# Performance work log

Measured on AMD Instinct MI355X. Metric: run time of the kernel, lower is better.

The kernel has to match this reference:

```python
import jax, jax.numpy as jnp
import numpy as np

N = 100000
E = 800000
IN_FEATS = 128
H_FEATS = 128
HEADS = 4
OUT = H_FEATS // HEADS  # 32
NEG_SLOPE = 0.2  # DGL GATConv default


def gat_conv(x, src, dst, W, attn_l, attn_r, bias):
    """DGL-style GATConv. x: [N, F_in] -> [N, HEADS, OUT]."""
    h = (x @ W).reshape(N, HEADS, OUT)                      # projected features
    el = jnp.sum(h * attn_l, axis=-1)                       # [N, H]
    er = jnp.sum(h * attn_r, axis=-1)                       # [N, H]
    e = jax.nn.leaky_relu(el[src] + er[dst], NEG_SLOPE)     # [E, H] edge logits
    # edge softmax over incoming edges of each dst node
    m = jax.ops.segment_max(e, dst, num_segments=N)          # [N, H]
    ex = jnp.exp(e - m[dst])                                 # [E, H]
    s = jax.ops.segment_sum(ex, dst, num_segments=N)         # [N, H]
    a = ex / s[dst]                                          # [E, H]
    msg = h[src] * a[:, :, None]                             # [E, H, OUT]
    out = jax.ops.segment_sum(msg, dst, num_segments=N)      # [N, H, OUT]
    return out + bias.reshape(1, HEADS, OUT)


def setup_inputs() -> dict:
    key = jax.random.key(0)
    ks = jax.random.split(key, 12)
    feat = jax.random.normal(ks[0], (N, IN_FEATS), dtype=jnp.float32)
    src = jax.random.randint(ks[1], (E,), 0, N)
    dst = jax.random.randint(ks[2], (E,), 0, N)
    s1 = 1.0 / np.sqrt(IN_FEATS)
    s2 = 1.0 / np.sqrt(H_FEATS)
    return {
        "feat": feat,
        "src": src,
        "dst": dst,
        "W1": jax.random.normal(ks[3], (IN_FEATS, HEADS * OUT), dtype=jnp.float32) * s1,
        "al1": jax.random.normal(ks[4], (HEADS, OUT), dtype=jnp.float32) * s2,
        "ar1": jax.random.normal(ks[5], (HEADS, OUT), dtype=jnp.float32) * s2,
        "b1": jnp.zeros((HEADS * OUT,), dtype=jnp.float32),
        "W2": jax.random.normal(ks[6], (H_FEATS, HEADS * OUT), dtype=jnp.float32) * s2,
        "al2": jax.random.normal(ks[7], (HEADS, OUT), dtype=jnp.float32) * s2,
        "ar2": jax.random.normal(ks[8], (HEADS, OUT), dtype=jnp.float32) * s2,
        "b2": jnp.zeros((HEADS * OUT,), dtype=jnp.float32),
    }


def reference(feat, src, dst, W1, al1, ar1, b1, W2, al2, ar2, b2):
    h = gat_conv(feat, src, dst, W1, al1, ar1, b1).reshape(N, H_FEATS)  # flatten(1)
    h = jax.nn.relu(h)
    h = gat_conv(h, src, dst, W2, al2, ar2, b2).mean(axis=1)            # mean over heads
    return h
```

## Files before the change

### kernel.cpp

```cpp
#include <hip/hip_runtime.h>
#include <math.h>

#define N_NODES 100000
#define N_EDGES 800000
#define NEG_SLOPE 0.2f
#define GEMM_BLOCKS 782
#define HIST_BLOCKS 3125
#define SCAN_BLOCKS 98

typedef __attribute__((ext_vector_type(8))) short short8;
typedef __attribute__((ext_vector_type(4))) float floatx4;

__device__ __forceinline__ float lrelu(float x) { return x > 0.f ? x : NEG_SLOPE * x; }

__device__ __forceinline__ unsigned bf16_rne(float f) {
    unsigned u = __float_as_uint(f);
    return (u + 0x7fffu + ((u >> 16) & 1u)) >> 16;
}
__device__ __forceinline__ unsigned bfpack(float lo, float hi) {
    return bf16_rne(lo) | (bf16_rne(hi) << 16);
}
__device__ __forceinline__ float bflo(unsigned p) { return __uint_as_float(p << 16); }
__device__ __forceinline__ float bfhi(unsigned p) { return __uint_as_float(p & 0xffff0000u); }

__global__ __launch_bounds__(256) void k_prep0(const float* __restrict__ W1,
                                               const float* __restrict__ al1,
                                               const float* __restrict__ ar1,
                                               const float* __restrict__ W2,
                                               const float* __restrict__ al2,
                                               const float* __restrict__ ar2,
                                               unsigned short* __restrict__ wt1,
                                               unsigned short* __restrict__ wt2,
                                               unsigned short* __restrict__ et1,
                                               unsigned short* __restrict__ et2,
                                               int* __restrict__ deg,
                                               int* __restrict__ done) {
    int b = blockIdx.x, tid = threadIdx.x;
    if (b < 128) {
        int t2 = b * 256 + tid;
        const float* W = (t2 < 16384) ? W1 : W2;
        unsigned short* wt = (t2 < 16384) ? wt1 : wt2;
        int t = t2 & 16383;
        int n = t >> 7, k = t & 127;
        wt[t] = (unsigned short)bf16_rne(W[k * 128 + n]);
    } else if (b < 130) {
        const float* W = (b == 128) ? W1 : W2;
        const float* al = (b == 128) ? al1 : al2;
        const float* ar = (b == 128) ? ar1 : ar2;
        unsigned short* et = (b == 128) ? et1 : et2;
        for (int o = tid * 8; o < tid * 8 + 8; o++) {
            int n = o >> 7, k = o & 127;
            float sacc = 0.f;
            if (n < 8) {
                const float* a = (n < 4) ? al : ar;
                int hh = n & 3;
                #pragma unroll 8
                for (int c = 0; c < 32; c++)
                    sacc += W[k * 128 + hh * 32 + c] * a[hh * 32 + c];
            }
            et[n * 128 + k] = (unsigned short)bf16_rne(sacc);
        }
    } else if (b < 228) {
        int i = (b - 130) * 1024 + tid * 4;
        if (i + 3 < N_NODES) *(int4*)&deg[i] = make_int4(0, 0, 0, 0);
        else { for (int j = i; j < N_NODES; j++) if (j >= 0) deg[j] = 0; }
    } else {
        if (tid < 64) done[tid] = 0;
    }
}

__device__ __forceinline__ void gemm_tile(int base, const void* __restrict__ Xv,
                                          const unsigned short* __restrict__ wt,
                                          const unsigned short* __restrict__ et,
                                          unsigned* __restrict__ Hb,
                                          float* __restrict__ EL,
                                          float* __restrict__ ER,
                                          int src_bf16,
                                          unsigned short* wsh,
                                          unsigned short* esh) {
    int tid = threadIdx.x;
    int w = tid >> 6, lane = tid & 63;
    int q = lane >> 4, nl = lane & 15;

    const uint4* wt4 = (const uint4*)wt;
    #pragma unroll
    for (int i = 0; i < 8; i++) {
        int idx = tid + i * 256;
        int rn = idx >> 4, c8 = idx & 15;
        int kc = c8 >> 2, qq = c8 & 3;
        int slot = rn * 128 + ((kc ^ ((rn >> 2) & 3)) * 4 + (qq ^ (rn & 3))) * 8;
        *(uint4*)&wsh[slot] = wt4[idx];
    }
    {
        const uint4* et4 = (const uint4*)et;
        int rn = tid >> 4, c8 = tid & 15;
        *(uint4*)&esh[rn * 136 + c8 * 8] = et4[tid];
    }

    short8 afr[2][4];
    int row0 = base + w * 32 + nl;
    if (!src_bf16) {
        const float4* X4 = (const float4*)Xv;
        #pragma unroll
        for (int rt = 0; rt < 2; rt++) {
            int rr = row0 + rt * 16; if (rr > N_NODES - 1) rr = N_NODES - 1;
            const float4* px = X4 + (size_t)rr * 32 + q * 2;
            #pragma unroll
            for (int kc = 0; kc < 4; kc++) {
                float4 u = px[kc * 8], v = px[kc * 8 + 1];
                short8 f;
                f[0] = (short)bf16_rne(u.x); f[1] = (short)bf16_rne(u.y);
                f[2] = (short)bf16_rne(u.z); f[3] = (short)bf16_rne(u.w);
                f[4] = (short)bf16_rne(v.x); f[5] = (short)bf16_rne(v.y);
                f[6] = (short)bf16_rne(v.z); f[7] = (short)bf16_rne(v.w);
                afr[rt][kc] = f;
            }
        }
    } else {
        const unsigned short* Xb = (const unsigned short*)Xv;
        #pragma unroll
        for (int rt = 0; rt < 2; rt++) {
            int rr = row0 + rt * 16; if (rr > N_NODES - 1) rr = N_NODES - 1;
            #pragma unroll
            for (int kc = 0; kc < 4; kc++)
                afr[rt][kc] = *(const short8*)(Xb + (size_t)rr * 128 + kc * 32 + q * 8);
        }
    }

    floatx4 acc[2][8];
    floatx4 acc_e[2];
    #pragma unroll
    for (int rt = 0; rt < 2; rt++) {
        acc_e[rt] = (floatx4){0.f, 0.f, 0.f, 0.f};
        #pragma unroll
        for (int ct = 0; ct < 8; ct++)
            acc[rt][ct] = (floatx4){0.f, 0.f, 0.f, 0.f};
    }

    __syncthreads();

    int sw_hi = (nl >> 2) & 3, sw_lo = nl & 3;
    #pragma unroll
    for (int ct = 0; ct < 8; ct++) {
        int rbase = (ct * 16 + nl) * 128;
        #pragma unroll
        for (int kc = 0; kc < 4; kc++) {
            short8 b = *(const short8*)&wsh[rbase + ((kc ^ sw_hi) * 4 + (q ^ sw_lo)) * 8];
            acc[0][ct] = __builtin_amdgcn_mfma_f32_16x16x32_bf16(afr[0][kc], b, acc[0][ct], 0, 0, 0);
            acc[1][ct] = __builtin_amdgcn_mfma_f32_16x16x32_bf16(afr[1][kc], b, acc[1][ct], 0, 0, 0);
        }
    }
    #pragma unroll
    for (int kc = 0; kc < 4; kc++) {
        short8 e8 = *(const short8*)&esh[nl * 136 + (kc * 4 + q) * 8];
        acc_e[0] = __builtin_amdgcn_mfma_f32_16x16x32_bf16(afr[0][kc], e8, acc_e[0], 0, 0, 0);
        acc_e[1] = __builtin_amdgcn_mfma_f32_16x16x32_bf16(afr[1][kc], e8, acc_e[1], 0, 0, 0);
    }

    #pragma unroll
    for (int rt = 0; rt < 2; rt++) {
        #pragma unroll
        for (int r = 0; r < 4; r++) {
            int row = base + w * 32 + rt * 16 + q * 4 + r;
            bool valid = row < N_NODES;
            unsigned* hrow = Hb + (size_t)row * 64;
            #pragma unroll
            for (int ct = 0; ct < 8; ct++) {
                float vlo = acc[rt][ct][r];
                float vhi = __shfl_down(vlo, 1);
                if (valid && !(nl & 1)) hrow[ct * 8 + (nl >> 1)] = bfpack(vlo, vhi);
            }
            if (valid && nl < 8) {
                float v = acc_e[rt][r];
                if (nl < 4) EL[row * 4 + nl] = v;
                else        ER[row * 4 + (nl & 3)] = v;
            }
        }
    }
}

__global__ __launch_bounds__(256) void k_gemm_hist(const float* __restrict__ feat,
                                                   const unsigned short* __restrict__ wt1,
                                                   const unsigned short* __restrict__ et1,
                                                   unsigned* __restrict__ Hb,
                                                   float* __restrict__ EL,
                                                   float* __restrict__ ER,
                                                   const int* __restrict__ dst,
                                                   int* __restrict__ deg) {
    __shared__ unsigned short wsh[128 * 128];
    __shared__ unsigned short esh[16 * 136];
    int b = blockIdx.x;
    if (b < GEMM_BLOCKS) {
        gemm_tile(b * 128, feat, wt1, et1, Hb, EL, ER, 0, wsh, esh);
    } else {
        int e = (b - GEMM_BLOCKS) * 256 + threadIdx.x;
        if (e < N_EDGES) atomicAdd(&deg[dst[e]], 1);
    }
}

__global__ __launch_bounds__(256) void k_gemm(const void* __restrict__ Xv,
                                              const unsigned short* __restrict__ wt,
                                              const unsigned short* __restrict__ et,
                                              unsigned* __restrict__ Hb,
                                              float* __restrict__ EL,
                                              float* __restrict__ ER,
                                              int src_bf16) {
    __shared__ unsigned short wsh[128 * 128];
    __shared__ unsigned short esh[16 * 136];
    gemm_tile(blockIdx.x * 128, Xv, wt, et, Hb, EL, ER, src_bf16, wsh, esh);
}

__global__ __launch_bounds__(256) void k_scan_scatter(const int* __restrict__ deg,
                                                      int* __restrict__ rs,
                                                      int* __restrict__ cursor,
                                                      int* __restrict__ bsums,
                                                      int* __restrict__ done,
                                                      const int* __restrict__ src,
                                                      const int* __restrict__ dst,
                                                      int* __restrict__ csr_src) {
    __shared__ int sd[256];
    int tid = threadIdx.x, b = blockIdx.x;
    int base = b * 1024 + tid * 4;
    int v0 = (base + 0 < N_NODES) ? deg[base + 0] : 0;
    int v1 = (base + 1 < N_NODES) ? deg[base + 1] : 0;
    int v2 = (base + 2 < N_NODES) ? deg[base + 2] : 0;
    int v3 = (base + 3 < N_NODES) ? deg[base + 3] : 0;
    int t = v0 + v1 + v2 + v3;
    sd[tid] = t;
    __syncthreads();
    int incl = t;
    for (int off = 1; off < 256; off <<= 1) {
        int x = (tid >= off) ? sd[tid - off] : 0;
        __syncthreads();
        incl += x;
        sd[tid] = incl;
        __syncthreads();
    }
    int excl = incl - t;

    if (tid == 255) {
        atomicExch(&bsums[b], incl);
        __threadfence();
        atomicAdd(&done[0], 1);
    }
    if (tid == 0) {
        while (atomicAdd(&done[0], 0) < SCAN_BLOCKS) { }
    }
    __syncthreads();

    int bv = (tid < b) ? atomicAdd(&bsums[tid], 0) : 0;
    __syncthreads();
    sd[tid] = bv;
    __syncthreads();
    for (int off = 128; off > 0; off >>= 1) {
        if (tid < off) sd[tid] += sd[tid + off];
        __syncthreads();
    }
    int boff = sd[0];

    int p0 = excl + boff;
    if (base + 0 < N_NODES) { rs[base + 0] = p0;                atomicExch(&cursor[base + 0], p0); }
    if (base + 1 < N_NODES) { rs[base + 1] = p0 + v0;           atomicExch(&cursor[base + 1], p0 + v0); }
    if (base + 2 < N_NODES) { rs[base + 2] = p0 + v0 + v1;      atomicExch(&cursor[base + 2], p0 + v0 + v1); }
    if (base + 3 < N_NODES) { rs[base + 3] = p0 + v0 + v1 + v2; atomicExch(&cursor[base + 3], p0 + v0 + v1 + v2); }
    if (b == 0 && tid == 0) rs[N_NODES] = N_EDGES;

    __threadfence();
    __syncthreads();
    if (tid == 0) {
        atomicAdd(&done[1], 1);
        while (atomicAdd(&done[1], 0) < SCAN_BLOCKS) { }
    }
    __syncthreads();

    const int stride = SCAN_BLOCKS * 256;
    int e = b * 256 + tid;
    while (e + 3 * stride < N_EDGES) {
        int d0 = dst[e];             int s0 = src[e];
        int d1 = dst[e + stride];    int s1 = src[e + stride];
        int d2 = dst[e + 2*stride];  int s2 = src[e + 2*stride];
        int d3 = dst[e + 3*stride];  int s3 = src[e + 3*stride];
        int q0 = atomicAdd(&cursor[d0], 1);
        int q1 = atomicAdd(&cursor[d1], 1);
        int q2 = atomicAdd(&cursor[d2], 1);
        int q3 = atomicAdd(&cursor[d3], 1);
        csr_src[q0] = s0;
        csr_src[q1] = s1;
        csr_src[q2] = s2;
        csr_src[q3] = s3;
        e += 4 * stride;
    }
    for (; e < N_EDGES; e += stride) {
        int d = dst[e];
        int p = atomicAdd(&cursor[d], 1);
        csr_src[p] = src[e];
    }
}

__global__ __launch_bounds__(256) void k_gather(const int* __restrict__ rs,
                                                const int* __restrict__ csr_src,
                                                const float* __restrict__ EL,
                                                const float* __restrict__ ER,
                                                const unsigned* __restrict__ Hb,
                                                const float* __restrict__ bias,
                                                void* __restrict__ out,
                                                int final_layer) {
    int wid = (blockIdx.x * blockDim.x + threadIdx.x) >> 6;
    int lane = threadIdx.x & 63;
    int g = lane >> 4, l16 = lane & 15;
    int h = l16 >> 2;
    int n0 = wid * 4;
    if (n0 >= N_NODES) return;
    int nend = min(n0 + 4, N_NODES);

    float bv[8];
    #pragma unroll
    for (int c = 0; c < 8; c++) bv[c] = bias[l16 * 8 + c];

    for (int n = n0; n < nend; n++) {
        int s = rs[n], e = rs[n + 1];
        float erh = ER[n * 4 + h];
        float acc[8];
        #pragma unroll
        for (int c = 0; c < 8; c++) acc[c] = 0.f;
        float sa = 0.f;

        for (int j = s; j < e; j += 8) {
            int j0 = j + g, j1 = j + 4 + g;
            uint4 p0 = make_uint4(0, 0, 0, 0), p1 = make_uint4(0, 0, 0, 0);
            float w0 = 0.f, w1 = 0.f;
            if (j0 < e) {
                int s0 = csr_src[j0];
                p0 = *(const uint4*)(Hb + (size_t)s0 * 64 + l16 * 4);
                w0 = __expf(lrelu(EL[s0 * 4 + h] + erh));
            }
            if (j1 < e) {
                int s1 = csr_src[j1];
                p1 = *(const uint4*)(Hb + (size_t)s1 * 64 + l16 * 4);
                w1 = __expf(lrelu(EL[s1 * 4 + h] + erh));
            }
            sa += w0 + w1;
            acc[0] = fmaf(bflo(p0.x), w0, acc[0]); acc[1] = fmaf(bfhi(p0.x), w0, acc[1]);
            acc[2] = fmaf(bflo(p0.y), w0, acc[2]); acc[3] = fmaf(bfhi(p0.y), w0, acc[3]);
            acc[4] = fmaf(bflo(p0.z), w0, acc[4]); acc[5] = fmaf(bfhi(p0.z), w0, acc[5]);
            acc[6] = fmaf(bflo(p0.w), w0, acc[6]); acc[7] = fmaf(bfhi(p0.w), w0, acc[7]);
            acc[0] = fmaf(bflo(p1.x), w1, acc[0]); acc[1] = fmaf(bfhi(p1.x), w1, acc[1]);
            acc[2] = fmaf(bflo(p1.y), w1, acc[2]); acc[3] = fmaf(bfhi(p1.y), w1, acc[3]);
            acc[4] = fmaf(bflo(p1.z), w1, acc[4]); acc[5] = fmaf(bfhi(p1.z), w1, acc[5]);
            acc[6] = fmaf(bflo(p1.w), w1, acc[6]); acc[7] = fmaf(bfhi(p1.w), w1, acc[7]);
        }

        #pragma unroll
        for (int c = 0; c < 8; c++) {
            acc[c] += __shfl_xor(acc[c], 16);
            acc[c] += __shfl_xor(acc[c], 32);
        }
        sa += __shfl_xor(sa, 16);
        sa += __shfl_xor(sa, 32);
        float inv = (e > s) ? 1.f / sa : 0.f;

        float r[8];
        #pragma unroll
        for (int c = 0; c < 8; c++) r[c] = acc[c] * inv + bv[c];

        if (!final_layer) {
            if (g == 0) {
                uint4 pk;
                pk.x = bfpack(fmaxf(r[0], 0.f), fmaxf(r[1], 0.f));
                pk.y = bfpack(fmaxf(r[2], 0.f), fmaxf(r[3], 0.f));
                pk.z = bfpack(fmaxf(r[4], 0.f), fmaxf(r[5], 0.f));
                pk.w = bfpack(fmaxf(r[6], 0.f), fmaxf(r[7], 0.f));
                *(uint4*)((unsigned*)out + (size_t)n * 64 + l16 * 4) = pk;
            }
        } else {
            #pragma unroll
            for (int c = 0; c < 8; c++) {
                r[c] += __shfl_xor(r[c], 4);
                r[c] += __shfl_xor(r[c], 8);
            }
            if (g == 0 && l16 < 4) {
                float* po = (float*)out + (size_t)n * 32 + l16 * 8;
                *(float4*)po = make_float4(0.25f * r[0], 0.25f * r[1], 0.25f * r[2], 0.25f * r[3]);
                *(float4*)(po + 4) = make_float4(0.25f * r[4], 0.25f * r[5], 0.25f * r[6], 0.25f * r[7]);
            }
        }
    }
}

extern "C" void kernel_launch(void* const* d_in, const int* in_sizes, int n_in,
                              void* d_out, int out_size, void* d_ws, size_t ws_size,
                              hipStream_t stream) {
    const float* feat = (const float*)d_in[0];
    const int* src = (const int*)d_in[1];
    const int* dst = (const int*)d_in[2];
    const float* W1 = (const float*)d_in[3];
    const float* al1 = (const float*)d_in[4];
    const float* ar1 = (const float*)d_in[5];
    const float* b1 = (const float*)d_in[6];
    const float* W2 = (const float*)d_in[7];
    const float* al2 = (const float*)d_in[8];
    const float* ar2 = (const float*)d_in[9];
    const float* b2 = (const float*)d_in[10];
    float* out = (float*)d_out;

    char* ws = (char*)d_ws;
    size_t off = 0;
    auto alloc = [&](size_t bytes) {
        void* p = ws + off;
        off += (bytes + 255) & ~(size_t)255;
        return p;
    };
    int* deg = (int*)alloc((size_t)N_NODES * 4);
    int* done = (int*)alloc(256);
    int* rs = (int*)alloc(((size_t)N_NODES + 1) * 4);
    int* cursor = (int*)alloc((size_t)N_NODES * 4);
    int* bsums = (int*)alloc(128 * 4);
    int* csr_src = (int*)alloc((size_t)N_EDGES * 4);
    unsigned* Hb = (unsigned*)alloc((size_t)N_NODES * 64 * 4);
    float* el = (float*)alloc((size_t)N_NODES * 4 * 4);
    float* er = (float*)alloc((size_t)N_NODES * 4 * 4);
    unsigned* out1b = (unsigned*)alloc((size_t)N_NODES * 64 * 4);
    unsigned short* wt1 = (unsigned short*)alloc(128 * 128 * 2);
    unsigned short* wt2 = (unsigned short*)alloc(128 * 128 * 2);
    unsigned short* et1 = (unsigned short*)alloc(16 * 128 * 2);
    unsigned short* et2 = (unsigned short*)alloc(16 * 128 * 2);

    int gat_blocks = (N_NODES + 15) / 16;

    k_prep0<<<229, 256, 0, stream>>>(W1, al1, ar1, W2, al2, ar2,
                                     wt1, wt2, et1, et2, deg, done);
    k_gemm_hist<<<GEMM_BLOCKS + HIST_BLOCKS, 256, 0, stream>>>(feat, wt1, et1, Hb, el, er,
                                                               dst, deg);
    k_scan_scatter<<<SCAN_BLOCKS, 256, 0, stream>>>(deg, rs, cursor, bsums, done,
                                                    src, dst, csr_src);
    k_gather<<<gat_blocks, 256, 0, stream>>>(rs, csr_src, el, er, Hb, b1, out1b, 0);
    k_gemm<<<GEMM_BLOCKS, 256, 0, stream>>>(out1b, wt2, et2, Hb, el, er, 1);
    k_gather<<<gat_blocks, 256, 0, stream>>>(rs, csr_src, el, er, Hb, b2, out, 1);
}
```

Baseline: 318.9 us.

## Record per-edge rank in histogram pass to drop scatter-phase atomics

The degree-histogram pass now stores each edge's atomicAdd return value as a 16-bit rank, and each thread handles four edges. The scatter phase then computes each CSR position as row_start[dst] + rank with plain loads instead of a second round of atomics on a cursor array, which also removes the cursor array. This trades the contended scatter atomics for an extra 1.6 MB rank write and read. It assumes no node has more than 65535 in-edges.

```diff
diff --git a/kernel.cpp b/kernel.cpp
--- a/kernel.cpp
+++ b/kernel.cpp
@@ -5,7 +5,7 @@
 #define N_EDGES 800000
 #define NEG_SLOPE 0.2f
 #define GEMM_BLOCKS 782
-#define HIST_BLOCKS 3125
+#define HIST4_BLOCKS 782
 #define SCAN_BLOCKS 98
 
 typedef __attribute__((ext_vector_type(8))) short short8;
@@ -186,15 +186,31 @@
                                                    float* __restrict__ EL,
                                                    float* __restrict__ ER,
                                                    const int* __restrict__ dst,
-                                                   int* __restrict__ deg) {
+                                                   int* __restrict__ deg,
+                                                   unsigned short* __restrict__ rank) {
     __shared__ unsigned short wsh[128 * 128];
     __shared__ unsigned short esh[16 * 136];
     int b = blockIdx.x;
     if (b < GEMM_BLOCKS) {
         gemm_tile(b * 128, feat, wt1, et1, Hb, EL, ER, 0, wsh, esh);
     } else {
-        int e = (b - GEMM_BLOCKS) * 256 + threadIdx.x;
-        if (e < N_EDGES) atomicAdd(&deg[dst[e]], 1);
+        int ebase = (b - GEMM_BLOCKS) * 1024 + threadIdx.x;
+        int d[4], c[4];
+        #pragma unroll
+        for (int k = 0; k < 4; k++) {
+            int e = ebase + k * 256;
+            d[k] = (e < N_EDGES) ? dst[e] : 0;
+        }
+        #pragma unroll
+        for (int k = 0; k < 4; k++) {
+            int e = ebase + k * 256;
+            c[k] = (e < N_EDGES) ? atomicAdd(&deg[d[k]], 1) : 0;
+        }
+        #pragma unroll
+        for (int k = 0; k < 4; k++) {
+            int e = ebase + k * 256;
+            if (e < N_EDGES) rank[e] = (unsigned short)c[k];
+        }
     }
 }
 
@@ -212,11 +228,11 @@
 
 __global__ __launch_bounds__(256) void k_scan_scatter(const int* __restrict__ deg,
                                                       int* __restrict__ rs,
-                                                      int* __restrict__ cursor,
                                                       int* __restrict__ bsums,
                                                       int* __restrict__ done,
                                                       const int* __restrict__ src,
                                                       const int* __restrict__ dst,
+                                                      const unsigned short* __restrict__ rank,
                                                       int* __restrict__ csr_src) {
     __shared__ int sd[256];
     int tid = threadIdx.x, b = blockIdx.x;
@@ -259,11 +275,11 @@
     int boff = sd[0];
 
     int p0 = excl + boff;
-    if (base + 0 < N_NODES) { rs[base + 0] = p0;                atomicExch(&cursor[base + 0], p0); }
-    if (base + 1 < N_NODES) { rs[base + 1] = p0 + v0;           atomicExch(&cursor[base + 1], p0 + v0); }
-    if (base + 2 < N_NODES) { rs[base + 2] = p0 + v0 + v1;      atomicExch(&cursor[base + 2], p0 + v0 + v1); }
-    if (base + 3 < N_NODES) { rs[base + 3] = p0 + v0 + v1 + v2; atomicExch(&cursor[base + 3], p0 + v0 + v1 + v2); }
-    if (b == 0 && tid == 0) rs[N_NODES] = N_EDGES;
+    if (base + 0 < N_NODES) atomicExch(&rs[base + 0], p0);
+    if (base + 1 < N_NODES) atomicExch(&rs[base + 1], p0 + v0);
+    if (base + 2 < N_NODES) atomicExch(&rs[base + 2], p0 + v0 + v1);
+    if (base + 3 < N_NODES) atomicExch(&rs[base + 3], p0 + v0 + v1 + v2);
+    if (b == 0 && tid == 0) atomicExch(&rs[N_NODES], N_EDGES);
 
     __threadfence();
     __syncthreads();
@@ -276,24 +292,19 @@
     const int stride = SCAN_BLOCKS * 256;
     int e = b * 256 + tid;
     while (e + 3 * stride < N_EDGES) {
-        int d0 = dst[e];             int s0 = src[e];
-        int d1 = dst[e + stride];    int s1 = src[e + stride];
-        int d2 = dst[e + 2*stride];  int s2 = src[e + 2*stride];
-        int d3 = dst[e + 3*stride];  int s3 = src[e + 3*stride];
-        int q0 = atomicAdd(&cursor[d0], 1);
-        int q1 = atomicAdd(&cursor[d1], 1);
-        int q2 = atomicAdd(&cursor[d2], 1);
-        int q3 = atomicAdd(&cursor[d3], 1);
-        csr_src[q0] = s0;
-        csr_src[q1] = s1;
-        csr_src[q2] = s2;
-        csr_src[q3] = s3;
+        int e1 = e + stride, e2 = e + 2 * stride, e3 = e + 3 * stride;
+        int d0 = dst[e],  d1 = dst[e1], d2 = dst[e2], d3 = dst[e3];
+        int s0 = src[e],  s1 = src[e1], s2 = src[e2], s3 = src[e3];
+        int r0 = rank[e], r1 = rank[e1], r2 = rank[e2], r3 = rank[e3];
+        int q0 = rs[d0], q1 = rs[d1], q2 = rs[d2], q3 = rs[d3];
+        csr_src[q0 + r0] = s0;
+        csr_src[q1 + r1] = s1;
+        csr_src[q2 + r2] = s2;
+        csr_src[q3 + r3] = s3;
         e += 4 * stride;
     }
     for (; e < N_EDGES; e += stride) {
-        int d = dst[e];
-        int p = atomicAdd(&cursor[d], 1);
-        csr_src[p] = src[e];
+        csr_src[rs[dst[e]] + rank[e]] = src[e];
     }
 }
 
@@ -413,8 +424,8 @@
     int* deg = (int*)alloc((size_t)N_NODES * 4);
     int* done = (int*)alloc(256);
     int* rs = (int*)alloc(((size_t)N_NODES + 1) * 4);
-    int* cursor = (int*)alloc((size_t)N_NODES * 4);
     int* bsums = (int*)alloc(128 * 4);
+    unsigned short* rank = (unsigned short*)alloc((size_t)HIST4_BLOCKS * 1024 * 2);
     int* csr_src = (int*)alloc((size_t)N_EDGES * 4);
     unsigned* Hb = (unsigned*)alloc((size_t)N_NODES * 64 * 4);
     float* el = (float*)alloc((size_t)N_NODES * 4 * 4);
@@ -429,10 +440,10 @@
 
     k_prep0<<<229, 256, 0, stream>>>(W1, al1, ar1, W2, al2, ar2,
                                      wt1, wt2, et1, et2, deg, done);
-    k_gemm_hist<<<GEMM_BLOCKS + HIST_BLOCKS, 256, 0, stream>>>(feat, wt1, et1, Hb, el, er,
-                                                               dst, deg);
-    k_scan_scatter<<<SCAN_BLOCKS, 256, 0, stream>>>(deg, rs, cursor, bsums, done,
-                                                    src, dst, csr_src);
+    k_gemm_hist<<<GEMM_BLOCKS + HIST4_BLOCKS, 256, 0, stream>>>(feat, wt1, et1, Hb, el, er,
+                                                                dst, deg, rank);
+    k_scan_scatter<<<SCAN_BLOCKS, 256, 0, stream>>>(deg, rs, bsums, done,
+                                                    src, dst, rank, csr_src);
     k_gather<<<gat_blocks, 256, 0, stream>>>(rs, csr_src, el, er, Hb, b1, out1b, 0);
     k_gemm<<<GEMM_BLOCKS, 256, 0, stream>>>(out1b, wt2, et2, Hb, el, er, 1);
     k_gather<<<gat_blocks, 256, 0, stream>>>(rs, csr_src, el, er, Hb, b2, out, 1);
```

After: 310.7 us. 1.03x faster.
